# Kernel tuning notes

Measured on AMD Instinct MI355X. Metric: run time of the kernel, lower is better.

Reference implementation:

```python
import jax, jax.numpy as jnp
import numpy as np

B, S, DIM = 2, 2048, 2048
NH, NKV = 16, 16
HD = 128            # constructor head_dim (full per-head dim, = 2 * self.head_dim)
HHD = HD // 2       # self.head_dim = per-stream dim = 64
ROPE_THETA = 10000.0
LAMBDA_INIT = 0.8 - 0.6 * float(np.exp(-0.3 * 0))  # block_id = 0 -> 0.2
EPS = 1e-5


def make_freq_cis(seq_len, dim, theta):
    # rotation matrices, shape (seq, dim//2, 2, 2): [[cos, -sin], [sin, cos]]
    inv = 1.0 / (theta ** (np.arange(0, dim, 2, dtype=np.float32) / dim))
    ang = np.arange(seq_len, dtype=np.float32)[:, None] * inv[None, :]
    cos, sin = np.cos(ang), np.sin(ang)
    fc = np.stack([np.stack([cos, -sin], -1), np.stack([sin, cos], -1)], -2)
    return jnp.asarray(fc, dtype=jnp.float32)


def setup_inputs() -> dict:
    key = jax.random.key(0)
    ks = jax.random.split(key, 9)
    std = DIM ** -0.5
    return {
        "x": jax.random.normal(ks[0], (B, S, DIM), jnp.float32),
        "freq_cis": make_freq_cis(S, HD, ROPE_THETA),
        "wq": jax.random.normal(ks[1], (NH * HD, DIM), jnp.float32) * std,
        "wk": jax.random.normal(ks[2], (NKV * HD, DIM), jnp.float32) * std,
        "wv": jax.random.normal(ks[3], (NKV * HD, DIM), jnp.float32) * std,
        "wo": jax.random.normal(ks[4], (DIM, NH * HD), jnp.float32) * std,
        "lambda_q1": jax.random.normal(ks[5], (HHD,), jnp.float32) * 0.1,
        "lambda_k1": jax.random.normal(ks[6], (HHD,), jnp.float32) * 0.1,
        "lambda_q2": jax.random.normal(ks[7], (HHD,), jnp.float32) * 0.1,
        "lambda_k2": jax.random.normal(ks[8], (HHD,), jnp.float32) * 0.1,
        "subln_w": jnp.ones((HD,), jnp.float32),
    }


def _rope(t, fc):
    # t: (b, s, h, d); fc: (s, d//2, 2, 2). Pairs (even, odd) rotated by 2x2 matrix.
    b, s, h, d = t.shape
    t2 = t.reshape(b, s, h, d // 2, 1, 2)
    out = (t2 * fc[None, :, None]).sum(-1)  # (b, s, h, d//2, 2)
    return out.reshape(b, s, h, d)


def _causal_attn(q, k, v):
    # q, k: (b, s, h, HHD); v: (b, s, h, HD). Flash-attn default scale = 1/sqrt(q head dim).
    scale = 1.0 / jnp.sqrt(jnp.asarray(q.shape[-1], q.dtype))
    scores = jnp.einsum('bqhd,bkhd->bhqk', q, k) * scale
    s = q.shape[1]
    causal = jnp.tril(jnp.ones((s, s), bool))
    scores = jnp.where(causal, scores, jnp.finfo(scores.dtype).min)
    p = jax.nn.softmax(scores, axis=-1)
    return jnp.einsum('bhqk,bkhd->bqhd', p, v)  # (b, s, h, HD)


def reference(x, freq_cis, wq, wk, wv, wo, lambda_q1, lambda_k1, lambda_q2, lambda_k2, subln_w):
    b, s, _ = x.shape
    xq = (x @ wq.T).reshape(b, s, NH, HD)
    xk = (x @ wk.T).reshape(b, s, NKV, HD)
    xv = (x @ wv.T).reshape(b, s, NKV, HD)
    xq = _rope(xq, freq_cis)
    xk = _rope(xk, freq_cis)
    if NKV != NH:  # GQA: repeat kv heads group-wise
        rep = NH // NKV
        xk = jnp.repeat(xk, rep, axis=2)
        xv = jnp.repeat(xv, rep, axis=2)
    # split each head into two differential streams of size HHD
    xq = xq.reshape(b, s, NH, 2, HHD)
    xk = xk.reshape(b, s, NH, 2, HHD)
    attn1 = _causal_attn(xq[:, :, :, 0], xk[:, :, :, 0], xv)
    attn2 = _causal_attn(xq[:, :, :, 1], xk[:, :, :, 1], xv)
    lam1 = jnp.exp(jnp.sum(lambda_q1 * lambda_k1))
    lam2 = jnp.exp(jnp.sum(lambda_q2 * lambda_k2))
    lam_full = lam1 - lam2 + LAMBDA_INIT
    attn = attn1 - lam_full * attn2              # (b, s, h, HD)
    attn = jnp.transpose(attn, (0, 2, 1, 3))     # faithful to torch .transpose(1, 2)
    ms = jnp.mean(jnp.square(attn), axis=-1, keepdims=True)
    attn = attn * jax.lax.rsqrt(ms + EPS) * subln_w  # RMSNorm(2*HHD)
    attn = attn * (1.0 - LAMBDA_INIT)
    # faithful to original: reshape (b, h, s, HD) row-major into (b, s, h*HD)
    attn = attn.reshape(b, s, NH * HD)
    return attn @ wo.T
```

## Files before the change

### kernel.cpp

```cpp
#include <hip/hip_runtime.h>

typedef unsigned short u16;
typedef unsigned int   u32;
typedef __attribute__((ext_vector_type(8))) short s16x8;
typedef __attribute__((ext_vector_type(4))) float f32x4;

constexpr int Bc = 2, Sc = 2048, DIMc = 2048, NHc = 16, HDc = 128, Tc = Bc * Sc;
constexpr float LAMBDA_INIT_C = 0.2f;

__device__ __forceinline__ u16 f2bf(float f) {
  union { float f; u32 u; } v; v.f = f;
  u32 r = v.u + 0x7fffu + ((v.u >> 16) & 1u);
  return (u16)(r >> 16);
}
__device__ __forceinline__ float bf2f(u16 b) {
  union { u32 u; float f; } v; v.u = ((u32)b) << 16;
  return v.f;
}
__device__ __forceinline__ f32x4 mfma16(s16x8 a, s16x8 b, f32x4 c) {
  return __builtin_amdgcn_mfma_f32_16x16x32_bf16(a, b, c, 0, 0, 0);
}

typedef const __attribute__((address_space(1))) u32 gq32;
typedef __attribute__((address_space(3))) u32 lq32;
__device__ __forceinline__ void cp16(const u16* g, u16* l) {
  __builtin_amdgcn_global_load_lds((gq32*)g, (lq32*)l, 16, 0, 0);
}

__global__ void cvt_all_kernel(const float* __restrict__ x,
                               const float* __restrict__ wq, const float* __restrict__ wk,
                               const float* __restrict__ wv, const float* __restrict__ wo,
                               u16* __restrict__ xb, u16* __restrict__ wb) {
  const int i = blockIdx.x * 256 + threadIdx.x;
  constexpr int NX = Tc * DIMc / 4;
  constexpr int PW = DIMc * DIMc / 4;
  float4 v; uint2* dst;
  if (i < NX) {
    v = ((const float4*)x)[i];
    dst = ((uint2*)xb) + i;
  } else {
    const int j = i - NX;
    const int which = j >> 20;
    const int jj = j & (PW - 1);
    const float* src = which == 0 ? wq : which == 1 ? wk : which == 2 ? wv : wo;
    v = ((const float4*)src)[jj];
    dst = ((uint2*)wb) + j;
  }
  union { u16 u[4]; uint2 p; } o;
  o.u[0] = f2bf(v.x); o.u[1] = f2bf(v.y); o.u[2] = f2bf(v.z); o.u[3] = f2bf(v.w);
  *dst = o.p;
}

template<int MODE>
__global__ __launch_bounds__(512, 2) void gemm8p(const u16* __restrict__ A,
                                                 const u16* __restrict__ Bw,
                                                 u16* __restrict__ Cb,
                                                 float* __restrict__ Cf) {
  constexpr int K = 2048, NT = K / 64;
  constexpr int BUF = 32768;
  __shared__ __align__(16) u16 L[2 * BUF];

  const int tid  = threadIdx.x;
  const int lane = tid & 63, w = tid >> 6;
  const int wm = w >> 2, wn = w & 3;
  const int l15 = lane & 15, quad = lane >> 4;

  const int mt   = gridDim.y;
  const int nwg  = gridDim.x * mt;
  const int flat = blockIdx.x * mt + blockIdx.y;
  const int swz  = (flat & 7) * (nwg >> 3) + (flat >> 3);
  const int nbase = (swz / mt) * 256;
  const int mbase = (swz % mt) * 256;

  const u16* Ag = A  + (size_t)mbase * K;
  const u16* Bg = Bw + (size_t)nbase * K;

  u32 soff[4], dlin[4];
#pragma unroll
  for (int l = 0; l < 4; l++) {
    const int n = l * 512 + tid;
    const int r = n >> 3;
    const u32 q = (u32)((n & 7) ^ (r & 7));
    soff[l] = (u32)r * K + q * 8;
    dlin[l] = (u32)n * 8;
  }

  auto stA = [&](int kt, int bb) {
#pragma unroll
    for (int l = 0; l < 4; l++)
      cp16(Ag + (size_t)kt * 64 + soff[l], L + bb + dlin[l]);
  };
  auto stB = [&](int kt, int bb) {
#pragma unroll
    for (int l = 0; l < 4; l++)
      cp16(Bg + (size_t)kt * 64 + soff[l], L + bb + 16384 + dlin[l]);
  };

  const int aB  = (wm * 128 + l15) * 64;
  const int bB  = 16384 + (wn * 64 + l15) * 64;
  const int xq0 = (quad ^ (l15 & 7)) << 3;

  f32x4 acc[8][4];
#pragma unroll
  for (int i = 0; i < 8; i++)
#pragma unroll
    for (int j = 0; j < 4; j++) acc[i][j] = (f32x4){0.f, 0.f, 0.f, 0.f};

  stB(0, 0); stA(0, 0); stB(1, BUF); stA(1, BUF);
  asm volatile("s_waitcnt vmcnt(8)" ::: "memory");
  asm volatile("s_barrier" ::: "memory");

  s16x8 a[4][2], b0[2][2], b1[2][2];

  for (int kt = 0; kt < NT; ++kt) {
    const int cb = (kt & 1) * BUF;
    const int tg = (kt + 2 < NT) ? kt + 2 : 0;

#pragma unroll
    for (int i = 0; i < 4; i++) {
      a[i][0] = *(const s16x8*)(L + cb + aB + i * 1024 + xq0);
      a[i][1] = *(const s16x8*)(L + cb + aB + i * 1024 + (xq0 ^ 32));
    }
#pragma unroll
    for (int j = 0; j < 2; j++) {
      b0[j][0] = *(const s16x8*)(L + cb + bB + j * 1024 + xq0);
      b0[j][1] = *(const s16x8*)(L + cb + bB + j * 1024 + (xq0 ^ 32));
    }
    asm volatile("s_barrier" ::: "memory");
    asm volatile("s_waitcnt lgkmcnt(0)" ::: "memory");
    __builtin_amdgcn_sched_barrier(0);
    __builtin_amdgcn_s_setprio(1);
#pragma unroll
    for (int i = 0; i < 4; i++)
#pragma unroll
      for (int j = 0; j < 2; j++) {
        acc[i][j] = mfma16(a[i][0], b0[j][0], acc[i][j]);
        acc[i][j] = mfma16(a[i][1], b0[j][1], acc[i][j]);
      }
    __builtin_amdgcn_s_setprio(0);
    asm volatile("s_barrier" ::: "memory");

#pragma unroll
    for (int j = 0; j < 2; j++) {
      b1[j][0] = *(const s16x8*)(L + cb + bB + (j + 2) * 1024 + xq0);
      b1[j][1] = *(const s16x8*)(L + cb + bB + (j + 2) * 1024 + (xq0 ^ 32));
    }
    asm volatile("s_barrier" ::: "memory");
    asm volatile("s_waitcnt lgkmcnt(0)" ::: "memory");
    __builtin_amdgcn_sched_barrier(0);
    __builtin_amdgcn_s_setprio(1);
#pragma unroll
    for (int i = 0; i < 4; i++)
#pragma unroll
      for (int j = 0; j < 2; j++) {
        acc[i][j + 2] = mfma16(a[i][0], b1[j][0], acc[i][j + 2]);
        acc[i][j + 2] = mfma16(a[i][1], b1[j][1], acc[i][j + 2]);
      }
    __builtin_amdgcn_s_setprio(0);
    asm volatile("s_barrier" ::: "memory");

#pragma unroll
    for (int i = 0; i < 4; i++) {
      a[i][0] = *(const s16x8*)(L + cb + aB + 4096 + i * 1024 + xq0);
      a[i][1] = *(const s16x8*)(L + cb + aB + 4096 + i * 1024 + (xq0 ^ 32));
    }
    stB(tg, cb);
    asm volatile("s_barrier" ::: "memory");
    asm volatile("s_waitcnt lgkmcnt(0)" ::: "memory");
    __builtin_amdgcn_sched_barrier(0);
    __builtin_amdgcn_s_setprio(1);
#pragma unroll
    for (int i = 0; i < 4; i++)
#pragma unroll
      for (int j = 0; j < 2; j++) {
        acc[i + 4][j + 2] = mfma16(a[i][0], b1[j][0], acc[i + 4][j + 2]);
        acc[i + 4][j + 2] = mfma16(a[i][1], b1[j][1], acc[i + 4][j + 2]);
      }
    __builtin_amdgcn_s_setprio(0);
    asm volatile("s_barrier" ::: "memory");

    stA(tg, cb);
    asm volatile("s_waitcnt vmcnt(8)" ::: "memory");
    asm volatile("s_barrier" ::: "memory");
    __builtin_amdgcn_sched_barrier(0);
    __builtin_amdgcn_s_setprio(1);
#pragma unroll
    for (int i = 0; i < 4; i++)
#pragma unroll
      for (int j = 0; j < 2; j++) {
        acc[i + 4][j] = mfma16(a[i][0], b0[j][0], acc[i + 4][j]);
        acc[i + 4][j] = mfma16(a[i][1], b0[j][1], acc[i + 4][j]);
      }
    __builtin_amdgcn_s_setprio(0);
    asm volatile("s_barrier" ::: "memory");
  }
  asm volatile("s_waitcnt vmcnt(0)" ::: "memory");

  if (MODE == 0) {
    const int which = nbase >> 11;
    const int ncol  = nbase & 2047;
    u16* Ob = Cb + (size_t)which * ((size_t)Tc * DIMc);
#pragma unroll
    for (int i = 0; i < 8; i++) {
      const int m0 = mbase + wm * 128 + i * 16 + quad * 4;
#pragma unroll
      for (int j = 0; j < 4; j++) {
        const int n0 = ncol + wn * 64 + j * 16 + l15;
#pragma unroll
        for (int r = 0; r < 4; r++)
          Ob[(size_t)(m0 + r) * 2048 + n0] = f2bf(acc[i][j][r]);
      }
    }
  } else {
#pragma unroll
    for (int i = 0; i < 8; i++) {
      const int m0 = mbase + wm * 128 + i * 16 + quad * 4;
#pragma unroll
      for (int j = 0; j < 4; j++) {
        const int n0 = nbase + wn * 64 + j * 16 + l15;
#pragma unroll
        for (int r = 0; r < 4; r++)
          Cf[(size_t)(m0 + r) * 2048 + n0] = acc[i][j][r];
      }
    }
  }
}

__global__ void prep_kernel(const u16* __restrict__ qg, const u16* __restrict__ kg,
                            const u16* __restrict__ vg, const float* __restrict__ fc,
                            u16* __restrict__ qr, u16* __restrict__ kr,
                            u16* __restrict__ vt) {
  __shared__ u16 tile[32][33];
  const int bid = blockIdx.x;
  if (bid < 32768) {
    const bool isq = bid < 16384;
    const u16* xg = isq ? qg : kg;
    u16* outp = isq ? qr : kr;
    const float scale = isq ? 0.125f : 1.0f;
    const int idx = (bid & 16383) * 256 + threadIdx.x;
    const int p = idx & 63;
    const int hh = (idx >> 6) & 15;
    const int tt = idx >> 10;
    const int s = tt & (Sc - 1);
    const int bb = tt >> 11;
    const float c  = fc[(size_t)(s * 64 + p) * 4 + 0] * scale;
    const float sn = fc[(size_t)(s * 64 + p) * 4 + 2] * scale;
    const u32 xp = *(const u32*)(xg + (size_t)tt * DIMc + hh * HDc + p * 2);
    const float x0 = bf2f((u16)xp), x1 = bf2f((u16)(xp >> 16));
    const u16 y0 = f2bf(c * x0 - sn * x1);
    const u16 y1 = f2bf(sn * x0 + c * x1);
    *(u32*)(outp + ((size_t)(bb * NHc + hh) * Sc + s) * HDc + p * 2) =
        (u32)y0 | ((u32)y1 << 16);
  } else {
    const int vb = bid - 32768;
    const int bh = vb >> 8;
    const int bb = bh >> 4, hh = bh & 15;
    const int rem = vb & 255;
    const int s0 = (rem & 63) * 32, d0 = (rem >> 6) * 32;
    const int tx = threadIdx.x & 31, ty = threadIdx.x >> 5;
#pragma unroll
    for (int pp = 0; pp < 4; pp++) {
      const int s = s0 + ty + pp * 8;
      tile[ty + pp * 8][tx] = vg[(size_t)(bb * Sc + s) * DIMc + hh * HDc + d0 + tx];
    }
    __syncthreads();
#pragma unroll
    for (int pp = 0; pp < 4; pp++) {
      const int d = d0 + ty + pp * 8;
      vt[((size_t)bh * HDc + d) * Sc + s0 + tx] = tile[tx][ty + pp * 8];
    }
  }
}

__global__ __launch_bounds__(256, 2) void diff_attn_kernel(
    const u16* __restrict__ qr, const u16* __restrict__ kr, const u16* __restrict__ vt,
    const float* __restrict__ lq1, const float* __restrict__ lk1,
    const float* __restrict__ lq2, const float* __restrict__ lk2,
    const float* __restrict__ subw, u16* __restrict__ Y) {
  __shared__ u16 KB[2][8192];
  __shared__ u16 VB[2][8192];

  const int h = blockIdx.y, b = blockIdx.z, jb = blockIdx.x;
  const int bh = b * NHc + h;
  const int tid = threadIdx.x;
  const int w = tid >> 6, lane = tid & 63;
  const int l15 = lane & 15, quad = lane >> 4;

  const u16* krb = kr + (size_t)bh * Sc * HDc;
  const u16* vtb = vt + (size_t)bh * HDc * Sc;

  float lp1 = lq1[lane] * lk1[lane];
  float lp2 = lq2[lane] * lk2[lane];
#pragma unroll
  for (int m = 32; m; m >>= 1) { lp1 += __shfl_xor(lp1, m); lp2 += __shfl_xor(lp2, m); }
  const float lam = __expf(lp1) - __expf(lp2) + LAMBDA_INIT_C;

  float wsub[8];
#pragma unroll
  for (int dn = 0; dn < 8; dn++) wsub[dn] = subw[dn * 16 + l15];

  size_t offK[4], offV[4];
  int dstO[4];
#pragma unroll
  for (int oo = 0; oo < 4; oo++) {
    const int n = w * 256 + oo * 64 + lane;
    const int s = n & 31, dblk = (n >> 5) & 15, sub = n >> 9;
    const int mkey = (s & 3) + ((s >> 2) & 3) * 8 + ((s >> 4) << 2);
    offK[oo] = (size_t)(sub * 32 + mkey) * HDc + dblk * 8;
    offV[oo] = (size_t)(n & 127) * Sc + (sub * 32 + ((n >> 7) & 3) * 8);
    dstO[oo] = n * 8;
  }

  for (int ph = 0; ph < 2; ph++) {
    const int t = ph ? (31 - jb) : jb;
    const int rowbase = t * 64 + w * 16;
    const int nc = t + 1;

    const u16* qp = qr + ((size_t)bh * Sc + rowbase + l15) * HDc + quad * 8;
    s16x8 qa[2][2];
    qa[0][0] = *(const s16x8*)(qp);
    qa[0][1] = *(const s16x8*)(qp + 32);
    qa[1][0] = *(const s16x8*)(qp + 64);
    qa[1][1] = *(const s16x8*)(qp + 96);

    f32x4 o[2][8];
#pragma unroll
    for (int st = 0; st < 2; st++)
#pragma unroll
      for (int dn = 0; dn < 8; dn++) o[st][dn] = (f32x4){0.f, 0.f, 0.f, 0.f};
    float lpart[2] = { 0.f, 0.f };

    __syncthreads();
#pragma unroll
    for (int oo = 0; oo < 4; oo++) cp16(krb + offK[oo], KB[0] + dstO[oo]);
#pragma unroll
    for (int oo = 0; oo < 4; oo++) cp16(vtb + offV[oo], VB[0] + dstO[oo]);

    for (int c = 0; c < nc; c++) {
      __syncthreads();
      if (c + 1 < nc) {
        const int kb1 = (c + 1) * 64;
        u16* Kn = KB[(c + 1) & 1];
        u16* Vn = VB[(c + 1) & 1];
#pragma unroll
        for (int oo = 0; oo < 4; oo++) cp16(krb + (size_t)kb1 * HDc + offK[oo], Kn + dstO[oo]);
#pragma unroll
        for (int oo = 0; oo < 4; oo++) cp16(vtb + offV[oo] + kb1, Vn + dstO[oo]);
      }
      const u16* Kb = KB[c & 1];
      const u16* Vb = VB[c & 1];
      const int kb = c * 64;
      const bool diag = (c == nc - 1);

#pragma unroll
      for (int sub = 0; sub < 2; sub++) {
        if (diag && sub == 1 && w < 2) continue;

        f32x4 sc[2][2];
#pragma unroll
        for (int st = 0; st < 2; st++)
#pragma unroll
          for (int kt = 0; kt < 2; kt++) sc[st][kt] = (f32x4){0.f, 0.f, 0.f, 0.f};
#pragma unroll
        for (int st = 0; st < 2; st++)
#pragma unroll
          for (int kh = 0; kh < 2; kh++) {
            const int base = sub * 512 + (st * 8 + kh * 4 + quad) * 32;
#pragma unroll
            for (int kt = 0; kt < 2; kt++) {
              const s16x8 kf = *(const s16x8*)(Kb + (size_t)(base + kt * 16 + l15) * 8);
              sc[st][kt] = mfma16(kf, qa[st][kh], sc[st][kt]);
            }
          }

        s16x8 pa[2];
#pragma unroll
        for (int st = 0; st < 2; st++) {
          float p[8];
#pragma unroll
          for (int kt = 0; kt < 2; kt++)
#pragma unroll
            for (int r = 0; r < 4; r++) p[kt * 4 + r] = __expf(sc[st][kt][r]);
          if (diag) {
            const int qrow = rowbase + l15;
            const int kb0 = kb + sub * 32 + quad * 8;
#pragma unroll
            for (int j8 = 0; j8 < 8; j8++)
              if (kb0 + j8 > qrow) p[j8] = 0.f;
          }
          float sm = 0.f;
#pragma unroll
          for (int j8 = 0; j8 < 8; j8++) sm += p[j8];
          lpart[st] += sm;
          union { u16 us[8]; s16x8 vv; } pk;
#pragma unroll
          for (int j8 = 0; j8 < 8; j8++) pk.us[j8] = f2bf(p[j8]);
          pa[st] = pk.vv;
        }

#pragma unroll
        for (int dn = 0; dn < 8; dn++) {
          const s16x8 vf =
              *(const s16x8*)(Vb + (size_t)(sub * 512 + quad * 128 + dn * 16 + l15) * 8);
          o[0][dn] = mfma16(pa[0], vf, o[0][dn]);
          o[1][dn] = mfma16(pa[1], vf, o[1][dn]);
        }
      }
    }

    float lL0 = lpart[0], lL1 = lpart[1];
    lL0 += __shfl_xor(lL0, 16); lL0 += __shfl_xor(lL0, 32);
    lL1 += __shfl_xor(lL1, 16); lL1 += __shfl_xor(lL1, 32);
    const float inv1 = 1.f / lL0;
    const float inv2 = lam / lL1;
    float i1C[4], i2C[4];
#pragma unroll
    for (int r = 0; r < 4; r++) {
      i1C[r] = __shfl(inv1, quad * 4 + r, 16);
      i2C[r] = __shfl(inv2, quad * 4 + r, 16);
    }
    float yv[8][4], ss[4] = { 0.f, 0.f, 0.f, 0.f };
#pragma unroll
    for (int dn = 0; dn < 8; dn++)
#pragma unroll
      for (int r = 0; r < 4; r++) {
        const float y = o[0][dn][r] * i1C[r] - o[1][dn][r] * i2C[r];
        yv[dn][r] = y;
        ss[r] += y * y;
      }
#pragma unroll
    for (int r = 0; r < 4; r++) {
#pragma unroll
      for (int mm = 1; mm < 16; mm <<= 1) ss[r] += __shfl_xor(ss[r], mm);
    }
    float scl[4];
#pragma unroll
    for (int r = 0; r < 4; r++) scl[r] = rsqrtf(ss[r] * (1.f / 128.f) + 1e-5f) * 0.8f;

    u16* yrow = Y + ((size_t)(b * Sc + h * 128 + t * 4 + w)) * 2048;
#pragma unroll
    for (int dn = 0; dn < 8; dn++)
#pragma unroll
      for (int r = 0; r < 4; r++)
        yrow[(quad * 4 + r) * 128 + dn * 16 + l15] = f2bf(yv[dn][r] * scl[r] * wsub[dn]);
  }
}

extern "C" void kernel_launch(void* const* d_in, const int* in_sizes, int n_in,
                              void* d_out, int out_size, void* d_ws, size_t ws_size,
                              hipStream_t stream) {
  const float* x    = (const float*)d_in[0];
  const float* fc   = (const float*)d_in[1];
  const float* wq   = (const float*)d_in[2];
  const float* wk   = (const float*)d_in[3];
  const float* wv   = (const float*)d_in[4];
  const float* wo   = (const float*)d_in[5];
  const float* lq1  = (const float*)d_in[6];
  const float* lk1  = (const float*)d_in[7];
  const float* lq2  = (const float*)d_in[8];
  const float* lk2  = (const float*)d_in[9];
  const float* subw = (const float*)d_in[10];
  float* out = (float*)d_out;

  char* ws = (char*)d_ws;
  constexpr size_t SZ_X  = (size_t)Tc * DIMc * 2;
  constexpr size_t SZ_W  = (size_t)DIMc * DIMc * 2;
  constexpr size_t SZ_T  = (size_t)Tc * DIMc * 2;
  u16* xb  = (u16*)(ws);
  u16* wqb = (u16*)(ws + SZ_X);
  u16* wob = (u16*)(ws + SZ_X + 3 * SZ_W);
  u16* qg  = (u16*)(ws + SZ_X + 4 * SZ_W);
  u16* kg  = (u16*)(ws + SZ_X + 4 * SZ_W + SZ_T);
  u16* vg  = (u16*)(ws + SZ_X + 4 * SZ_W + 2 * SZ_T);
  u16* qr  = (u16*)(ws + SZ_X + 4 * SZ_W + 3 * SZ_T);
  u16* kr  = (u16*)(ws + SZ_X + 4 * SZ_W + 4 * SZ_T);
  u16* vt  = (u16*)(ws + SZ_X + 4 * SZ_W + 5 * SZ_T);
  u16* Y   = (u16*)(ws + SZ_X + 4 * SZ_W + 6 * SZ_T);

  cvt_all_kernel<<<(Tc * DIMc / 4 + 4 * DIMc * DIMc / 4) / 256, 256, 0, stream>>>(
      x, wq, wk, wv, wo, xb, wqb);

  gemm8p<0><<<dim3(DIMc * 3 / 256, Tc / 256), 512, 0, stream>>>(
      xb, wqb, qg, nullptr);

  prep_kernel<<<16384 + 16384 + 8192, 256, 0, stream>>>(qg, kg, vg, fc, qr, kr, vt);

  diff_attn_kernel<<<dim3(16, NHc, Bc), 256, 0, stream>>>(
      qr, kr, vt, lq1, lk1, lq2, lk2, subw, Y);

  gemm8p<1><<<dim3(DIMc / 256, Tc / 256), 512, 0, stream>>>(
      Y, wob, nullptr, out);
}
```

Measured before the change: 439.3 us.

## Parameterize GEMM M-tile and restructure k-loop pipeline; use 128-row tiles for output projection

Templates the bf16 GEMM on the M tile size and rewrites the inner k-loop so each phase covers one k-half across all B columns. A is now prefetched one stage ahead and B two stages ahead, with different wait counts. The output projection switches to 128-row tiles, doubling its workgroup count from 128 to 256 so more CUs are busy on the 256-CU part. The trade-off is less data reuse per tile and a changed pipeline ordering that could expose LDS or global latency.

Result: faster. 416.8 us (-5.1%).

```diff
diff --git a/kernel.cpp b/kernel.cpp
--- a/kernel.cpp
+++ b/kernel.cpp
@@ -26,6 +26,10 @@
 __device__ __forceinline__ void cp16(const u16* g, u16* l) {
   __builtin_amdgcn_global_load_lds((gq32*)g, (lq32*)l, 16, 0, 0);
 }
+
+#define BAR()    asm volatile("s_barrier" ::: "memory")
+#define LGKM0()  asm volatile("s_waitcnt lgkmcnt(0)" ::: "memory")
+#define VMC(n)   asm volatile("s_waitcnt vmcnt(" #n ")" ::: "memory")
 
 __global__ void cvt_all_kernel(const float* __restrict__ x,
                                const float* __restrict__ wq, const float* __restrict__ wk,
@@ -51,13 +55,16 @@
   *dst = o.p;
 }
 
-template<int MODE>
+template<int MODE, int BM>
 __global__ __launch_bounds__(512, 2) void gemm8p(const u16* __restrict__ A,
                                                  const u16* __restrict__ Bw,
                                                  u16* __restrict__ Cb,
                                                  float* __restrict__ Cf) {
   constexpr int K = 2048, NT = K / 64;
-  constexpr int BUF = 32768;
+  constexpr int AF  = BM / 32;
+  constexpr int AU  = BM * 64;
+  constexpr int ALD = BM / 64;
+  constexpr int BUF = AU + 16384;
   __shared__ __align__(16) u16 L[2 * BUF];
 
   const int tid  = threadIdx.x;
@@ -70,129 +77,122 @@
   const int flat = blockIdx.x * mt + blockIdx.y;
   const int swz  = (flat & 7) * (nwg >> 3) + (flat >> 3);
   const int nbase = (swz / mt) * 256;
-  const int mbase = (swz % mt) * 256;
+  const int mbase = (swz % mt) * BM;
 
   const u16* Ag = A  + (size_t)mbase * K;
   const u16* Bg = Bw + (size_t)nbase * K;
 
-  u32 soff[4], dlin[4];
+  u32 soffA[ALD], dlinA[ALD], soffB[4], dlinB[4];
+#pragma unroll
+  for (int l = 0; l < ALD; l++) {
+    const int n = l * 512 + tid;
+    const int r = n >> 3;
+    const u32 q = (u32)((n & 7) ^ (r & 7));
+    soffA[l] = (u32)r * K + q * 8;
+    dlinA[l] = (u32)n * 8;
+  }
 #pragma unroll
   for (int l = 0; l < 4; l++) {
     const int n = l * 512 + tid;
     const int r = n >> 3;
     const u32 q = (u32)((n & 7) ^ (r & 7));
-    soff[l] = (u32)r * K + q * 8;
-    dlin[l] = (u32)n * 8;
+    soffB[l] = (u32)r * K + q * 8;
+    dlinB[l] = (u32)(AU + n * 8);
   }
 
   auto stA = [&](int kt, int bb) {
 #pragma unroll
-    for (int l = 0; l < 4; l++)
-      cp16(Ag + (size_t)kt * 64 + soff[l], L + bb + dlin[l]);
+    for (int l = 0; l < ALD; l++)
+      cp16(Ag + (size_t)kt * 64 + soffA[l], L + bb + dlinA[l]);
   };
   auto stB = [&](int kt, int bb) {
 #pragma unroll
     for (int l = 0; l < 4; l++)
-      cp16(Bg + (size_t)kt * 64 + soff[l], L + bb + 16384 + dlin[l]);
+      cp16(Bg + (size_t)kt * 64 + soffB[l], L + bb + dlinB[l]);
   };
 
-  const int aB  = (wm * 128 + l15) * 64;
-  const int bB  = 16384 + (wn * 64 + l15) * 64;
+  const int aB  = (wm * (BM / 2) + l15) * 64;
+  const int bB  = AU + (wn * 64 + l15) * 64;
   const int xq0 = (quad ^ (l15 & 7)) << 3;
 
-  f32x4 acc[8][4];
-#pragma unroll
-  for (int i = 0; i < 8; i++)
+  f32x4 acc[AF][4];
+#pragma unroll
+  for (int i = 0; i < AF; i++)
 #pragma unroll
     for (int j = 0; j < 4; j++) acc[i][j] = (f32x4){0.f, 0.f, 0.f, 0.f};
 
-  stB(0, 0); stA(0, 0); stB(1, BUF); stA(1, BUF);
-  asm volatile("s_waitcnt vmcnt(8)" ::: "memory");
-  asm volatile("s_barrier" ::: "memory");
-
-  s16x8 a[4][2], b0[2][2], b1[2][2];
+  stB(0, 0); stA(0, 0); stB(1, BUF);
+  VMC(4);
+  BAR();
+
+  s16x8 a[AF], b[4];
 
   for (int kt = 0; kt < NT; ++kt) {
     const int cb = (kt & 1) * BUF;
-    const int tg = (kt + 2 < NT) ? kt + 2 : 0;
-
-#pragma unroll
-    for (int i = 0; i < 4; i++) {
-      a[i][0] = *(const s16x8*)(L + cb + aB + i * 1024 + xq0);
-      a[i][1] = *(const s16x8*)(L + cb + aB + i * 1024 + (xq0 ^ 32));
-    }
-#pragma unroll
-    for (int j = 0; j < 2; j++) {
-      b0[j][0] = *(const s16x8*)(L + cb + bB + j * 1024 + xq0);
-      b0[j][1] = *(const s16x8*)(L + cb + bB + j * 1024 + (xq0 ^ 32));
-    }
-    asm volatile("s_barrier" ::: "memory");
-    asm volatile("s_waitcnt lgkmcnt(0)" ::: "memory");
+    const int nb = BUF - cb;
+    const int tgA = (kt + 1 < NT) ? kt + 1 : 0;
+    const int tgB = (kt + 2 < NT) ? kt + 2 : 0;
+
+#pragma unroll
+    for (int j = 0; j < 4; j++)
+      b[j] = *(const s16x8*)(L + cb + bB + j * 1024 + xq0);
+#pragma unroll
+    for (int i = 0; i < AF / 2; i++)
+      a[i] = *(const s16x8*)(L + cb + aB + i * 1024 + xq0);
+    stA(tgA, nb);
+    BAR(); LGKM0();
     __builtin_amdgcn_sched_barrier(0);
     __builtin_amdgcn_s_setprio(1);
 #pragma unroll
-    for (int i = 0; i < 4; i++)
-#pragma unroll
-      for (int j = 0; j < 2; j++) {
-        acc[i][j] = mfma16(a[i][0], b0[j][0], acc[i][j]);
-        acc[i][j] = mfma16(a[i][1], b0[j][1], acc[i][j]);
-      }
+    for (int i = 0; i < AF / 2; i++)
+#pragma unroll
+      for (int j = 0; j < 4; j++) acc[i][j] = mfma16(a[i], b[j], acc[i][j]);
     __builtin_amdgcn_s_setprio(0);
-    asm volatile("s_barrier" ::: "memory");
-
-#pragma unroll
-    for (int j = 0; j < 2; j++) {
-      b1[j][0] = *(const s16x8*)(L + cb + bB + (j + 2) * 1024 + xq0);
-      b1[j][1] = *(const s16x8*)(L + cb + bB + (j + 2) * 1024 + (xq0 ^ 32));
-    }
-    asm volatile("s_barrier" ::: "memory");
-    asm volatile("s_waitcnt lgkmcnt(0)" ::: "memory");
+    BAR();
+
+#pragma unroll
+    for (int i = AF / 2; i < AF; i++)
+      a[i] = *(const s16x8*)(L + cb + aB + i * 1024 + xq0);
+    BAR(); LGKM0();
     __builtin_amdgcn_sched_barrier(0);
     __builtin_amdgcn_s_setprio(1);
 #pragma unroll
-    for (int i = 0; i < 4; i++)
-#pragma unroll
-      for (int j = 0; j < 2; j++) {
-        acc[i][j + 2] = mfma16(a[i][0], b1[j][0], acc[i][j + 2]);
-        acc[i][j + 2] = mfma16(a[i][1], b1[j][1], acc[i][j + 2]);
-      }
+    for (int i = AF / 2; i < AF; i++)
+#pragma unroll
+      for (int j = 0; j < 4; j++) acc[i][j] = mfma16(a[i], b[j], acc[i][j]);
     __builtin_amdgcn_s_setprio(0);
-    asm volatile("s_barrier" ::: "memory");
-
-#pragma unroll
-    for (int i = 0; i < 4; i++) {
-      a[i][0] = *(const s16x8*)(L + cb + aB + 4096 + i * 1024 + xq0);
-      a[i][1] = *(const s16x8*)(L + cb + aB + 4096 + i * 1024 + (xq0 ^ 32));
-    }
-    stB(tg, cb);
-    asm volatile("s_barrier" ::: "memory");
-    asm volatile("s_waitcnt lgkmcnt(0)" ::: "memory");
+    BAR();
+
+#pragma unroll
+    for (int j = 0; j < 4; j++)
+      b[j] = *(const s16x8*)(L + cb + bB + j * 1024 + (xq0 ^ 32));
+#pragma unroll
+    for (int i = 0; i < AF / 2; i++)
+      a[i] = *(const s16x8*)(L + cb + aB + i * 1024 + (xq0 ^ 32));
+    BAR(); LGKM0();
     __builtin_amdgcn_sched_barrier(0);
     __builtin_amdgcn_s_setprio(1);
 #pragma unroll
-    for (int i = 0; i < 4; i++)
-#pragma unroll
-      for (int j = 0; j < 2; j++) {
-        acc[i + 4][j + 2] = mfma16(a[i][0], b1[j][0], acc[i + 4][j + 2]);
-        acc[i + 4][j + 2] = mfma16(a[i][1], b1[j][1], acc[i + 4][j + 2]);
-      }
+    for (int i = 0; i < AF / 2; i++)
+#pragma unroll
+      for (int j = 0; j < 4; j++) acc[i][j] = mfma16(a[i], b[j], acc[i][j]);
     __builtin_amdgcn_s_setprio(0);
-    asm volatile("s_barrier" ::: "memory");
-
-    stA(tg, cb);
-    asm volatile("s_waitcnt vmcnt(8)" ::: "memory");
-    asm volatile("s_barrier" ::: "memory");
+    BAR();
+
+#pragma unroll
+    for (int i = AF / 2; i < AF; i++)
+      a[i] = *(const s16x8*)(L + cb + aB + i * 1024 + (xq0 ^ 32));
+    stB(tgB, cb);
+    VMC(4);
+    BAR(); LGKM0();
     __builtin_amdgcn_sched_barrier(0);
     __builtin_amdgcn_s_setprio(1);
 #pragma unroll
-    for (int i = 0; i < 4; i++)
-#pragma unroll
-      for (int j = 0; j < 2; j++) {
-        acc[i + 4][j] = mfma16(a[i][0], b0[j][0], acc[i + 4][j]);
-        acc[i + 4][j] = mfma16(a[i][1], b0[j][1], acc[i + 4][j]);
-      }
+    for (int i = AF / 2; i < AF; i++)
+#pragma unroll
+      for (int j = 0; j < 4; j++) acc[i][j] = mfma16(a[i], b[j], acc[i][j]);
     __builtin_amdgcn_s_setprio(0);
-    asm volatile("s_barrier" ::: "memory");
+    BAR();
   }
   asm volatile("s_waitcnt vmcnt(0)" ::: "memory");
 
@@ -201,8 +201,8 @@
     const int ncol  = nbase & 2047;
     u16* Ob = Cb + (size_t)which * ((size_t)Tc * DIMc);
 #pragma unroll
-    for (int i = 0; i < 8; i++) {
-      const int m0 = mbase + wm * 128 + i * 16 + quad * 4;
+    for (int i = 0; i < AF; i++) {
+      const int m0 = mbase + wm * (BM / 2) + i * 16 + quad * 4;
 #pragma unroll
       for (int j = 0; j < 4; j++) {
         const int n0 = ncol + wn * 64 + j * 16 + l15;
@@ -213,8 +213,8 @@
     }
   } else {
 #pragma unroll
-    for (int i = 0; i < 8; i++) {
-      const int m0 = mbase + wm * 128 + i * 16 + quad * 4;
+    for (int i = 0; i < AF; i++) {
+      const int m0 = mbase + wm * (BM / 2) + i * 16 + quad * 4;
 #pragma unroll
       for (int j = 0; j < 4; j++) {
         const int n0 = nbase + wn * 64 + j * 16 + l15;
@@ -480,7 +480,7 @@
   cvt_all_kernel<<<(Tc * DIMc / 4 + 4 * DIMc * DIMc / 4) / 256, 256, 0, stream>>>(
       x, wq, wk, wv, wo, xb, wqb);
 
-  gemm8p<0><<<dim3(DIMc * 3 / 256, Tc / 256), 512, 0, stream>>>(
+  gemm8p<0, 256><<<dim3(DIMc * 3 / 256, Tc / 256), 512, 0, stream>>>(
       xb, wqb, qg, nullptr);
 
   prep_kernel<<<16384 + 16384 + 8192, 256, 0, stream>>>(qg, kg, vg, fc, qr, kr, vt);
@@ -488,6 +488,6 @@
   diff_attn_kernel<<<dim3(16, NHc, Bc), 256, 0, stream>>>(
       qr, kr, vt, lq1, lk1, lq2, lk2, subw, Y);
 
-  gemm8p<1><<<dim3(DIMc / 256, Tc / 256), 512, 0, stream>>>(
+  gemm8p<1, 128><<<dim3(DIMc / 256, Tc / 128), 512, 0, stream>>>(
       Y, wob, nullptr, out);
 }
```
